# Kernel tuning notes

Hardware: AMD Instinct MI355X
Metric: run time of the kernel (lower is better)

## Reference

```python
import jax, jax.numpy as jnp
import numpy as np

EPS = 1e-15
PROJ_EPS = 1e-05


def project_hyp_vec(x):
    # clamp squared norm from below at 1 - PROJ_EPS (torch.clamp with min only)
    norm = jnp.sum(x * x, axis=-1, keepdims=True)
    return x * (1.0 - PROJ_EPS) / jnp.maximum(norm, 1.0 - PROJ_EPS)


def atanh(x):
    return 0.5 * jnp.log((1.0 + x) / (1.0 - x))


def mob_add(u, v):
    v = v + EPS
    norm_uv = 2.0 * jnp.sum(u * v, axis=-1, keepdims=True)
    norm_u = jnp.sum(u * u, axis=-1, keepdims=True)
    norm_v = jnp.sum(v * v, axis=-1, keepdims=True)
    denom = 1.0 + norm_uv + norm_v * norm_u
    result = (1.0 + norm_uv + norm_v) / denom * u + (1.0 - norm_u) / denom * v
    return project_hyp_vec(result)


def mob_mat_mul(M, x):
    x = project_hyp_vec(x)
    Mx = x @ M                                   # [B, H]
    Mx_norm = jnp.linalg.norm(Mx + EPS, axis=-1, keepdims=True)
    x_norm = jnp.linalg.norm(x + EPS, axis=-1, keepdims=True)
    return project_hyp_vec(jnp.tanh(Mx_norm / x_norm * atanh(x_norm)) / Mx_norm * Mx)


def setup_inputs() -> dict:
    key = jax.random.key(0)
    k_in, k_w, k_u = jax.random.split(key, 3)
    B, S, I, H = 256, 512, 256, 256
    inputs = jax.random.normal(k_in, (B, S, I), dtype=jnp.float32) * 0.1
    k = (1.0 / H) ** 0.5
    w = jax.random.uniform(k_w, (H, H), minval=-k, maxval=k, dtype=jnp.float32)
    u = jax.random.uniform(k_u, (I, H), minval=-k, maxval=k, dtype=jnp.float32)
    b = jnp.zeros((H,), dtype=jnp.float32)
    return {"inputs": inputs, "w": w, "u": u, "b": b}


def reference(inputs, w, u, b):
    B, S, I = inputs.shape
    H = w.shape[0]

    def step(h, x):
        Wh = mob_mat_mul(w, h)          # [B, H]
        Ux = mob_mat_mul(u, x)          # [B, H]
        h_new = mob_add(mob_add(Wh, Ux), b)
        return h_new, h_new

    h0 = jnp.zeros((B, H), dtype=inputs.dtype)
    _, outs = jax.lax.scan(step, h0, jnp.swapaxes(inputs, 0, 1))  # [S, B, H]
    return jnp.swapaxes(outs, 0, 1)  # [B, S, H]
```

## Files before the change

kernel.cpp:

```cpp
#include <hip/hip_runtime.h>

#define EPSV 1e-15f
#define PEPS 1e-5f

typedef float v2f __attribute__((ext_vector_type(2)));

__device__ __forceinline__ float frcp(float x) { return __builtin_amdgcn_rcpf(x); }
__device__ __forceinline__ float fexp2(float x) { return __builtin_amdgcn_exp2f(x); }
__device__ __forceinline__ float flog2(float x) { return __builtin_amdgcn_logf(x); }
__device__ __forceinline__ float projscale(float n2) {
  return n2 > (1.f - PEPS) ? (1.f - PEPS) * frcp(n2) : 1.f;
}

template <int CTRL>
__device__ __forceinline__ float dppadd(float x) {
  int y = __builtin_amdgcn_update_dpp(0, __float_as_int(x), CTRL, 0xF, 0xF, true);
  return x + __int_as_float(y);
}
__device__ __forceinline__ float wave_sum(float x) {
  x = dppadd<0x111>(x);
  x = dppadd<0x112>(x);
  x = dppadd<0x114>(x);
  x = dppadd<0x118>(x);
  x = dppadd<0x142>(x);
  x = dppadd<0x143>(x);
  return __int_as_float(__builtin_amdgcn_readlane(__float_as_int(x), 63));
}

__global__ __launch_bounds__(256) void ux_kernel(
    const float* __restrict__ x, const float* __restrict__ u,
    const float* __restrict__ bvec, float* __restrict__ out,
    float4* __restrict__ vstat, int use_vstat)
{
  __shared__ __align__(16) float xsT[256][36];

  const int tid = threadIdx.x;
  const int lane = tid & 63, wv = tid >> 6;
  const long long base = (long long)blockIdx.x * 32;

  #pragma unroll
  for (int k4 = 0; k4 < 8; ++k4) {
    float t0 = x[(base + k4 * 4 + 0) * 256 + tid];
    float t1 = x[(base + k4 * 4 + 1) * 256 + tid];
    float t2 = x[(base + k4 * 4 + 2) * 256 + tid];
    float t3 = x[(base + k4 * 4 + 3) * 256 + tid];
    float4 v; v.x = t0; v.y = t1; v.z = t2; v.w = t3;
    *reinterpret_cast<float4*>(&xsT[tid][k4 * 4]) = v;
  }
  __syncthreads();

  float4 bb = *reinterpret_cast<const float4*>(&bvec[4 * lane]);
  bb.x += EPSV; bb.y += EPSV; bb.z += EPSV; bb.w += EPSV;
  float S_vbrow = wave_sum(bb.x + bb.y + bb.z + bb.w);

  float s1[8], s2[8];
  #pragma unroll
  for (int r = 0; r < 8; ++r) { s1[r] = 0.f; s2[r] = 0.f; }
  #pragma unroll
  for (int c = 0; c < 4; ++c) {
    const int i = lane + 64 * c;
    float4 xa = *reinterpret_cast<const float4*>(&xsT[i][8 * wv]);
    float4 xb = *reinterpret_cast<const float4*>(&xsT[i][8 * wv + 4]);
    s1[0] += xa.x; s2[0] += xa.x * xa.x;
    s1[1] += xa.y; s2[1] += xa.y * xa.y;
    s1[2] += xa.z; s2[2] += xa.z * xa.z;
    s1[3] += xa.w; s2[3] += xa.w * xa.w;
    s1[4] += xb.x; s2[4] += xb.x * xb.x;
    s1[5] += xb.y; s2[5] += xb.y * xb.y;
    s1[6] += xb.z; s2[6] += xb.z * xb.z;
    s1[7] += xb.w; s2[7] += xb.w * xb.w;
  }
  float rs[8], xnr[8];
  #pragma unroll
  for (int r = 0; r < 8; ++r) {
    float a = wave_sum(s1[r]);
    float b2 = wave_sum(s2[r]);
    float sc = projscale(b2);
    rs[r] = sc;
    xnr[r] = sqrtf(sc * sc * b2 + 2.f * sc * EPSV * a + 256.f * EPSV * EPSV);
  }

  float4 acc[8];
  #pragma unroll
  for (int r = 0; r < 8; ++r) { acc[r].x = 0.f; acc[r].y = 0.f; acc[r].z = 0.f; acc[r].w = 0.f; }
  #pragma unroll 2
  for (int i = 0; i < 256; ++i) {
    float4 uv = *reinterpret_cast<const float4*>(&u[i * 256 + 4 * lane]);
    float4 xa = *reinterpret_cast<const float4*>(&xsT[i][8 * wv]);
    float4 xb = *reinterpret_cast<const float4*>(&xsT[i][8 * wv + 4]);
    acc[0].x += uv.x * xa.x; acc[0].y += uv.y * xa.x; acc[0].z += uv.z * xa.x; acc[0].w += uv.w * xa.x;
    acc[1].x += uv.x * xa.y; acc[1].y += uv.y * xa.y; acc[1].z += uv.z * xa.y; acc[1].w += uv.w * xa.y;
    acc[2].x += uv.x * xa.z; acc[2].y += uv.y * xa.z; acc[2].z += uv.z * xa.z; acc[2].w += uv.w * xa.z;
    acc[3].x += uv.x * xa.w; acc[3].y += uv.y * xa.w; acc[3].z += uv.z * xa.w; acc[3].w += uv.w * xa.w;
    acc[4].x += uv.x * xb.x; acc[4].y += uv.y * xb.x; acc[4].z += uv.z * xb.x; acc[4].w += uv.w * xb.x;
    acc[5].x += uv.x * xb.y; acc[5].y += uv.y * xb.y; acc[5].z += uv.z * xb.y; acc[5].w += uv.w * xb.y;
    acc[6].x += uv.x * xb.z; acc[6].y += uv.y * xb.z; acc[6].z += uv.z * xb.z; acc[6].w += uv.w * xb.z;
    acc[7].x += uv.x * xb.w; acc[7].y += uv.y * xb.w; acc[7].z += uv.z * xb.w; acc[7].w += uv.w * xb.w;
  }

  #pragma unroll
  for (int r = 0; r < 8; ++r) {
    float t1 = wave_sum(acc[r].x + acc[r].y + acc[r].z + acc[r].w);
    float t2 = wave_sum(acc[r].x * acc[r].x + acc[r].y * acc[r].y +
                        acc[r].z * acc[r].z + acc[r].w * acc[r].w);
    float t3 = wave_sum(acc[r].x * bb.x + acc[r].y * bb.y + acc[r].z * bb.z + acc[r].w * bb.w);
    float Sm  = rs[r] * t1;
    float Sm2 = rs[r] * rs[r] * t2;
    float mxn = sqrtf(Sm2 + 2.f * EPSV * Sm + 256.f * EPSV * EPSV);
    float xn = xnr[r];
    float at = 0.34657359f * flog2((1.f + xn) * frcp(1.f - xn));
    float arg = mxn * frcp(xn) * at;
    float e2 = fexp2(arg * 2.8853902f);
    float th = 1.f - 2.f * frcp(e2 + 1.f);
    float g = th * frcp(mxn);
    float fs = g * projscale(g * g * Sm2) * rs[r];
    float4 o;
    o.x = fs * acc[r].x + EPSV; o.y = fs * acc[r].y + EPSV;
    o.z = fs * acc[r].z + EPSV; o.w = fs * acc[r].w + EPSV;
    reinterpret_cast<float4*>(out)[(base + 8 * wv + r) * 64 + lane] = o;
    if (use_vstat && lane == 0) {
      float Sv  = fs * t1 + 256.f * EPSV;
      float Sv2 = fs * fs * t2 + 2.f * EPSV * fs * t1 + 256.f * EPSV * EPSV;
      float Svb = fs * t3 + EPSV * S_vbrow;
      vstat[base + 8 * wv + r] = float4{Sv, Sv2, Svb, 0.f};
    }
  }
}

template <int NR>
__device__ __forceinline__ void load_w(const float* __restrict__ w, int rb, int lane, v2f* wr) {
  #pragma unroll
  for (int r = 0; r < NR; ++r) {
    float4 t = *reinterpret_cast<const float4*>(&w[(rb + r) * 256 + 4 * lane]);
    asm volatile("" : "+v"(t.x), "+v"(t.y), "+v"(t.z), "+v"(t.w));
    wr[2 * r]     = v2f{t.x, t.y};
    wr[2 * r + 1] = v2f{t.z, t.w};
  }
}

template <int NR>
__device__ __forceinline__ void mv_pq(const v2f* wr, const float* mxp, const float* vp,
                                      float4& P, float4& Q) {
  v2f pl{0.f, 0.f}, ph{0.f, 0.f}, ql{0.f, 0.f}, qh{0.f, 0.f};
  #pragma unroll
  for (int i = 0; i < NR / 4; ++i) {
    float4 h4 = *reinterpret_cast<const float4*>(mxp + 4 * i);
    float4 u4 = *reinterpret_cast<const float4*>(vp + 4 * i);
    pl += wr[8 * i + 0] * h4.x; ph += wr[8 * i + 1] * h4.x;
    pl += wr[8 * i + 2] * h4.y; ph += wr[8 * i + 3] * h4.y;
    pl += wr[8 * i + 4] * h4.z; ph += wr[8 * i + 5] * h4.z;
    pl += wr[8 * i + 6] * h4.w; ph += wr[8 * i + 7] * h4.w;
    ql += wr[8 * i + 0] * u4.x; qh += wr[8 * i + 1] * u4.x;
    ql += wr[8 * i + 2] * u4.y; qh += wr[8 * i + 3] * u4.y;
    ql += wr[8 * i + 4] * u4.z; qh += wr[8 * i + 5] * u4.z;
    ql += wr[8 * i + 6] * u4.w; qh += wr[8 * i + 7] * u4.w;
  }
  P = float4{pl.x, pl.y, ph.x, ph.y};
  Q = float4{ql.x, ql.y, qh.x, qh.y};
}

__global__ __launch_bounds__(512, 1) void rnn_kernel(
    const float* __restrict__ w, const float* __restrict__ bvec,
    float* __restrict__ out, const float4* __restrict__ vstat, int S, int use_vstat)
{
  __shared__ __align__(16) float mx_lds[256];
  __shared__ __align__(16) float v_lds[2][256];
  __shared__ __align__(16) float pP[8][256];
  __shared__ __align__(16) float pQ[8][256];

  const int tid = threadIdx.x;
  const int lane = tid & 63;
  const int wv = tid >> 6;

  const long long rb4 = (long long)blockIdx.x * S * 64;
  const long long vsbase = (long long)blockIdx.x * S;
  const float4* outv = reinterpret_cast<const float4*>(out);
  float4* outw = reinterpret_cast<float4*>(out);
  const float4 zero4{0.f, 0.f, 0.f, 0.f};

  if (wv == 0) {
    v2f wr0[8];
    load_w<4>(w, 0, lane, wr0);

    float4 vb4 = *reinterpret_cast<const float4*>(&bvec[4 * lane]);
    vb4.x += EPSV; vb4.y += EPSV; vb4.z += EPSV; vb4.w += EPSV;
    float S_vb  = wave_sum(vb4.x + vb4.y + vb4.z + vb4.w);
    float S_vb2 = wave_sum(vb4.x * vb4.x + vb4.y * vb4.y + vb4.z * vb4.z + vb4.w * vb4.w);

    reinterpret_cast<float4*>(mx_lds)[lane] = zero4;
    reinterpret_cast<float4*>(v_lds[0])[lane] = vb4;
    __syncthreads();

    {
      float4 P, Q; mv_pq<4>(wr0, &mx_lds[0], &v_lds[0][0], P, Q);
      *reinterpret_cast<float4*>(&pP[0][4 * lane]) = P;
      *reinterpret_cast<float4*>(&pQ[0][4 * lane]) = Q;
    }
    __syncthreads();

    float4 Wvb4 = zero4;
    #pragma unroll
    for (int k = 0; k < 8; ++k) {
      float4 qq = *reinterpret_cast<const float4*>(&pQ[k][4 * lane]);
      Wvb4.x += qq.x; Wvb4.y += qq.y; Wvb4.z += qq.z; Wvb4.w += qq.w;
    }
    float4 vA = outv[rb4 + lane];
    float4 vB = outv[rb4 + 64 + lane];
    float4 sA = zero4, sB = zero4;
    if (use_vstat) { sA = vstat[vsbase]; sB = vstat[vsbase + 1]; }
    reinterpret_cast<float4*>(v_lds[0])[lane] = vA;
    __syncthreads();

    float4 m4 = zero4;
    float S_h = 0.f, S_h2 = 0.f;

    for (int t = 0; t < S; ++t) {
      const int b = t & 1;
      float4 v4 = vA;

      float S_Mx  = wave_sum(m4.x + m4.y + m4.z + m4.w);
      float S_Mx2 = wave_sum(m4.x * m4.x + m4.y * m4.y + m4.z * m4.z + m4.w * m4.w);
      float S_Mxv = wave_sum(m4.x * v4.x + m4.y * v4.y + m4.z * v4.z + m4.w * v4.w);
      float S_Mxb = wave_sum(m4.x * vb4.x + m4.y * vb4.y + m4.z * vb4.z + m4.w * vb4.w);
      float S_v, S_v2, S_vvb;
      if (use_vstat) { S_v = sA.x; S_v2 = sA.y; S_vvb = sA.z; }
      else {
        S_v   = wave_sum(v4.x + v4.y + v4.z + v4.w);
        S_v2  = wave_sum(v4.x * v4.x + v4.y * v4.y + v4.z * v4.z + v4.w * v4.w);
        S_vvb = wave_sum(v4.x * vb4.x + v4.y * vb4.y + v4.z * vb4.z + v4.w * vb4.w);
      }

      float s_hp = projscale(S_h2);
      float xn = sqrtf(s_hp * s_hp * S_h2 + 2.f * s_hp * EPSV * S_h + 256.f * EPSV * EPSV);
      float mxn = sqrtf(S_Mx2 + 2.f * EPSV * S_Mx + 256.f * EPSV * EPSV);
      float at = 0.34657359f * flog2((1.f + xn) * frcp(1.f - xn));
      float arg = mxn * frcp(xn) * at;
      float e2 = fexp2(arg * 2.8853902f);
      float th = 1.f - 2.f * frcp(e2 + 1.f);
      float g = th * frcp(mxn);
      float beta = g * projscale(g * g * S_Mx2);

      float nuv = 2.f * beta * S_Mxv;
      float nu  = beta * beta * S_Mx2;
      float nv  = S_v2;
      float rden = frcp(1.f + nuv + nv * nu);
      float cA = (1.f + nuv + nv) * rden;
      float cB = (1.f - nu) * rden;
      float cAb = cA * beta;
      float S_r1  = cAb * S_Mx + cB * S_v;
      float S_r12 = cAb * cAb * S_Mx2 + 2.f * cAb * cB * S_Mxv + cB * cB * S_v2;
      float S_r1b = cAb * S_Mxb + cB * S_vvb;
      float s1p = projscale(S_r12);
      float S_U = s1p * S_r1, S_U2 = s1p * s1p * S_r12, S_Ub = s1p * S_r1b;

      float nuv2 = 2.f * S_Ub;
      float rden2 = frcp(1.f + nuv2 + S_vb2 * S_U2);
      float dA = (1.f + nuv2 + S_vb2) * rden2;
      float dB = (1.f - S_U2) * rden2;
      float S_hn  = dA * S_U + dB * S_vb;
      float S_hn2 = dA * dA * S_U2 + 2.f * dA * dB * S_Ub + dB * dB * S_vb2;
      float s2p = projscale(S_hn2);

      float km = s2p * dA * s1p * cAb;
      float kv = s2p * dA * s1p * cB;
      float kb = s2p * dB;

      float4 hn{km * m4.x + kv * v4.x + kb * vb4.x,
                km * m4.y + kv * v4.y + kb * vb4.y,
                km * m4.z + kv * v4.z + kb * vb4.z,
                km * m4.w + kv * v4.w + kb * vb4.w};
      outw[rb4 + (long long)t * 64 + lane] = hn;

      S_h  = s2p * S_hn;
      S_h2 = s2p * s2p * S_hn2;
      float snextp = projscale(S_h2);

      if (t + 1 < S) reinterpret_cast<float4*>(v_lds[(t + 1) & 1])[lane] = vB;
      float4 vC = vB, sC = sB;
      if (t + 2 < S) {
        vC = outv[rb4 + (long long)(t + 2) * 64 + lane];
        if (use_vstat) sC = vstat[vsbase + t + 2];
      }

      {
        float4 P, Q; mv_pq<4>(wr0, &mx_lds[0], &v_lds[b][0], P, Q);
        *reinterpret_cast<float4*>(&pP[0][4 * lane]) = P;
        *reinterpret_cast<float4*>(&pQ[0][4 * lane]) = Q;
      }
      __syncthreads();

      float4 Pc = zero4, Qc = zero4;
      #pragma unroll
      for (int k = 0; k < 8; ++k) {
        float4 pp = *reinterpret_cast<const float4*>(&pP[k][4 * lane]);
        float4 qq = *reinterpret_cast<const float4*>(&pQ[k][4 * lane]);
        Pc.x += pp.x; Pc.y += pp.y; Pc.z += pp.z; Pc.w += pp.w;
        Qc.x += qq.x; Qc.y += qq.y; Qc.z += qq.z; Qc.w += qq.w;
      }
      m4.x = snextp * (km * Pc.x + kv * Qc.x + kb * Wvb4.x);
      m4.y = snextp * (km * Pc.y + kv * Qc.y + kb * Wvb4.y);
      m4.z = snextp * (km * Pc.z + kv * Qc.z + kb * Wvb4.z);
      m4.w = snextp * (km * Pc.w + kv * Qc.w + kb * Wvb4.w);
      reinterpret_cast<float4*>(mx_lds)[lane] = m4;
      __syncthreads();

      vA = vB; vB = vC; sA = sB; sB = sC;
    }
  } else {
    const int rb = 4 + (wv - 1) * 36;
    v2f wrk[72];
    load_w<36>(w, rb, lane, wrk);
    __syncthreads();
    {
      float4 P, Q; mv_pq<36>(wrk, &mx_lds[rb], &v_lds[0][rb], P, Q);
      *reinterpret_cast<float4*>(&pP[wv][4 * lane]) = P;
      *reinterpret_cast<float4*>(&pQ[wv][4 * lane]) = Q;
    }
    __syncthreads();
    __syncthreads();

    for (int t = 0; t < S; ++t) {
      const int b = t & 1;
      float4 P, Q;
      mv_pq<36>(wrk, &mx_lds[rb], &v_lds[b][rb], P, Q);
      *reinterpret_cast<float4*>(&pP[wv][4 * lane]) = P;
      *reinterpret_cast<float4*>(&pQ[wv][4 * lane]) = Q;
      __syncthreads();
      __syncthreads();
    }
  }
}

extern "C" void kernel_launch(void* const* d_in, const int* in_sizes, int n_in,
                              void* d_out, int out_size, void* d_ws, size_t ws_size,
                              hipStream_t stream) {
  const float* x = (const float*)d_in[0];
  const float* w = (const float*)d_in[1];
  const float* u = (const float*)d_in[2];
  const float* b = (const float*)d_in[3];
  float* out = (float*)d_out;

  const int nrows = in_sizes[0] / 256;
  const int S = 512;
  const int B = nrows / S;

  const int use_vstat = (ws_size >= (size_t)nrows * 16) ? 1 : 0;
  float4* vstat = (float4*)d_ws;

  ux_kernel<<<nrows / 32, 256, 0, stream>>>(x, u, b, out, vstat, use_vstat);
  rnn_kernel<<<B, 512, 0, stream>>>(w, b, out, vstat, S, use_vstat);
}
```

Baseline: 906.2 us.

## Split recurrent matvec across 16 waves and offload input prefetch to a helper wave

The recurrent kernel grows from 8 to 16 waves per block (1024 threads). Each worker wave now holds 16 or 20 rows of W in registers instead of 36, and wave 0 holds 8 rows, which shortens the per-step matvec critical path. Prefetching the next input rows into LDS moves from the serial wave 0 to wave 1, so wave 0 now reads v from LDS. The cost is a wider barrier across 16 waves, a 16-way partial-sum reduction in wave 0, and doubled LDS for partials.

```diff
diff --git a/kernel.cpp b/kernel.cpp
--- a/kernel.cpp
+++ b/kernel.cpp
@@ -159,14 +159,22 @@
   Q = float4{ql.x, ql.y, qh.x, qh.y};
 }
 
-__global__ __launch_bounds__(512, 1) void rnn_kernel(
+__device__ __forceinline__ int row_base(int wv) {
+  if (wv == 0) return 0;
+  if (wv <= 13) return 8 + (wv - 1) * 16;
+  return 216 + (wv - 14) * 20;
+}
+
+__global__ __launch_bounds__(1024)
+__attribute__((amdgpu_waves_per_eu(4, 4)))
+void rnn_kernel(
     const float* __restrict__ w, const float* __restrict__ bvec,
     float* __restrict__ out, const float4* __restrict__ vstat, int S, int use_vstat)
 {
   __shared__ __align__(16) float mx_lds[256];
   __shared__ __align__(16) float v_lds[2][256];
-  __shared__ __align__(16) float pP[8][256];
-  __shared__ __align__(16) float pQ[8][256];
+  __shared__ __align__(16) float pP[16][256];
+  __shared__ __align__(16) float pQ[16][256];
 
   const int tid = threadIdx.x;
   const int lane = tid & 63;
@@ -179,8 +187,8 @@
   const float4 zero4{0.f, 0.f, 0.f, 0.f};
 
   if (wv == 0) {
-    v2f wr0[8];
-    load_w<4>(w, 0, lane, wr0);
+    v2f wr[16];
+    load_w<8>(w, 0, lane, wr);
 
     float4 vb4 = *reinterpret_cast<const float4*>(&bvec[4 * lane]);
     vb4.x += EPSV; vb4.y += EPSV; vb4.z += EPSV; vb4.w += EPSV;
@@ -192,7 +200,7 @@
     __syncthreads();
 
     {
-      float4 P, Q; mv_pq<4>(wr0, &mx_lds[0], &v_lds[0][0], P, Q);
+      float4 P, Q; mv_pq<8>(wr, &mx_lds[0], &v_lds[0][0], P, Q);
       *reinterpret_cast<float4*>(&pP[0][4 * lane]) = P;
       *reinterpret_cast<float4*>(&pQ[0][4 * lane]) = Q;
     }
@@ -200,15 +208,12 @@
 
     float4 Wvb4 = zero4;
     #pragma unroll
-    for (int k = 0; k < 8; ++k) {
+    for (int k = 0; k < 16; ++k) {
       float4 qq = *reinterpret_cast<const float4*>(&pQ[k][4 * lane]);
       Wvb4.x += qq.x; Wvb4.y += qq.y; Wvb4.z += qq.z; Wvb4.w += qq.w;
     }
-    float4 vA = outv[rb4 + lane];
-    float4 vB = outv[rb4 + 64 + lane];
-    float4 sA = zero4, sB = zero4;
-    if (use_vstat) { sA = vstat[vsbase]; sB = vstat[vsbase + 1]; }
-    reinterpret_cast<float4*>(v_lds[0])[lane] = vA;
+    float sAx = 0.f, sAy = 0.f, sAz = 0.f;
+    if (use_vstat) { float4 s = vstat[vsbase]; sAx = s.x; sAy = s.y; sAz = s.z; }
     __syncthreads();
 
     float4 m4 = zero4;
@@ -216,14 +221,17 @@
 
     for (int t = 0; t < S; ++t) {
       const int b = t & 1;
-      float4 v4 = vA;
+      float nsx = 0.f, nsy = 0.f, nsz = 0.f;
+      if (use_vstat && t + 1 < S) { float4 s = vstat[vsbase + t + 1]; nsx = s.x; nsy = s.y; nsz = s.z; }
+
+      float4 v4 = *reinterpret_cast<const float4*>(&v_lds[b][4 * lane]);
 
       float S_Mx  = wave_sum(m4.x + m4.y + m4.z + m4.w);
       float S_Mx2 = wave_sum(m4.x * m4.x + m4.y * m4.y + m4.z * m4.z + m4.w * m4.w);
       float S_Mxv = wave_sum(m4.x * v4.x + m4.y * v4.y + m4.z * v4.z + m4.w * v4.w);
       float S_Mxb = wave_sum(m4.x * vb4.x + m4.y * vb4.y + m4.z * vb4.z + m4.w * vb4.w);
       float S_v, S_v2, S_vvb;
-      if (use_vstat) { S_v = sA.x; S_v2 = sA.y; S_vvb = sA.z; }
+      if (use_vstat) { S_v = sAx; S_v2 = sAy; S_vvb = sAz; }
       else {
         S_v   = wave_sum(v4.x + v4.y + v4.z + v4.w);
         S_v2  = wave_sum(v4.x * v4.x + v4.y * v4.y + v4.z * v4.z + v4.w * v4.w);
@@ -275,15 +283,8 @@
       S_h2 = s2p * s2p * S_hn2;
       float snextp = projscale(S_h2);
 
-      if (t + 1 < S) reinterpret_cast<float4*>(v_lds[(t + 1) & 1])[lane] = vB;
-      float4 vC = vB, sC = sB;
-      if (t + 2 < S) {
-        vC = outv[rb4 + (long long)(t + 2) * 64 + lane];
-        if (use_vstat) sC = vstat[vsbase + t + 2];
-      }
-
       {
-        float4 P, Q; mv_pq<4>(wr0, &mx_lds[0], &v_lds[b][0], P, Q);
+        float4 P, Q; mv_pq<8>(wr, &mx_lds[0], &v_lds[b][0], P, Q);
         *reinterpret_cast<float4*>(&pP[0][4 * lane]) = P;
         *reinterpret_cast<float4*>(&pQ[0][4 * lane]) = Q;
       }
@@ -291,7 +292,7 @@
 
       float4 Pc = zero4, Qc = zero4;
       #pragma unroll
-      for (int k = 0; k < 8; ++k) {
+      for (int k = 0; k < 16; ++k) {
         float4 pp = *reinterpret_cast<const float4*>(&pP[k][4 * lane]);
         float4 qq = *reinterpret_cast<const float4*>(&pQ[k][4 * lane]);
         Pc.x += pp.x; Pc.y += pp.y; Pc.z += pp.z; Pc.w += pp.w;
@@ -304,29 +305,80 @@
       reinterpret_cast<float4*>(mx_lds)[lane] = m4;
       __syncthreads();
 
-      vA = vB; vB = vC; sA = sB; sB = sC;
-    }
-  } else {
-    const int rb = 4 + (wv - 1) * 36;
-    v2f wrk[72];
-    load_w<36>(w, rb, lane, wrk);
+      sAx = nsx; sAy = nsy; sAz = nsz;
+    }
+  } else if (wv == 1) {
+    v2f wr[32];
+    const int rb = row_base(1);
+    load_w<16>(w, rb, lane, wr);
+
+    float4 vA = outv[rb4 + lane];
+    float4 vB = outv[rb4 + 64 + lane];
+    float4 vC = outv[rb4 + 128 + lane];
     __syncthreads();
     {
-      float4 P, Q; mv_pq<36>(wrk, &mx_lds[rb], &v_lds[0][rb], P, Q);
-      *reinterpret_cast<float4*>(&pP[wv][4 * lane]) = P;
-      *reinterpret_cast<float4*>(&pQ[wv][4 * lane]) = Q;
-    }
-    __syncthreads();
+      float4 P, Q; mv_pq<16>(wr, &mx_lds[rb], &v_lds[0][rb], P, Q);
+      *reinterpret_cast<float4*>(&pP[1][4 * lane]) = P;
+      *reinterpret_cast<float4*>(&pQ[1][4 * lane]) = Q;
+    }
+    __syncthreads();
+    reinterpret_cast<float4*>(v_lds[0])[lane] = vA;
     __syncthreads();
 
     for (int t = 0; t < S; ++t) {
       const int b = t & 1;
       float4 P, Q;
-      mv_pq<36>(wrk, &mx_lds[rb], &v_lds[b][rb], P, Q);
-      *reinterpret_cast<float4*>(&pP[wv][4 * lane]) = P;
-      *reinterpret_cast<float4*>(&pQ[wv][4 * lane]) = Q;
-      __syncthreads();
-      __syncthreads();
+      mv_pq<16>(wr, &mx_lds[rb], &v_lds[b][rb], P, Q);
+      *reinterpret_cast<float4*>(&pP[1][4 * lane]) = P;
+      *reinterpret_cast<float4*>(&pQ[1][4 * lane]) = Q;
+      if (t + 1 < S) reinterpret_cast<float4*>(v_lds[(t + 1) & 1])[lane] = vB;
+      vB = vC;
+      if (t + 3 < S) vC = outv[rb4 + (long long)(t + 3) * 64 + lane];
+      __syncthreads();
+      __syncthreads();
+    }
+  } else {
+    const int rb = row_base(wv);
+    if (wv >= 14) {
+      v2f wr[40];
+      load_w<20>(w, rb, lane, wr);
+      __syncthreads();
+      {
+        float4 P, Q; mv_pq<20>(wr, &mx_lds[rb], &v_lds[0][rb], P, Q);
+        *reinterpret_cast<float4*>(&pP[wv][4 * lane]) = P;
+        *reinterpret_cast<float4*>(&pQ[wv][4 * lane]) = Q;
+      }
+      __syncthreads();
+      __syncthreads();
+      for (int t = 0; t < S; ++t) {
+        const int b = t & 1;
+        float4 P, Q;
+        mv_pq<20>(wr, &mx_lds[rb], &v_lds[b][rb], P, Q);
+        *reinterpret_cast<float4*>(&pP[wv][4 * lane]) = P;
+        *reinterpret_cast<float4*>(&pQ[wv][4 * lane]) = Q;
+        __syncthreads();
+        __syncthreads();
+      }
+    } else {
+      v2f wr[32];
+      load_w<16>(w, rb, lane, wr);
+      __syncthreads();
+      {
+        float4 P, Q; mv_pq<16>(wr, &mx_lds[rb], &v_lds[0][rb], P, Q);
+        *reinterpret_cast<float4*>(&pP[wv][4 * lane]) = P;
+        *reinterpret_cast<float4*>(&pQ[wv][4 * lane]) = Q;
+      }
+      __syncthreads();
+      __syncthreads();
+      for (int t = 0; t < S; ++t) {
+        const int b = t & 1;
+        float4 P, Q;
+        mv_pq<16>(wr, &mx_lds[rb], &v_lds[b][rb], P, Q);
+        *reinterpret_cast<float4*>(&pP[wv][4 * lane]) = P;
+        *reinterpret_cast<float4*>(&pQ[wv][4 * lane]) = Q;
+        __syncthreads();
+        __syncthreads();
+      }
     }
   }
 }
@@ -348,5 +400,5 @@
   float4* vstat = (float4*)d_ws;
 
   ux_kernel<<<nrows / 32, 256, 0, stream>>>(x, u, b, out, vstat, use_vstat);
-  rnn_kernel<<<B, 512, 0, stream>>>(w, b, out, vstat, S, use_vstat);
-}
+  rnn_kernel<<<B, 1024, 0, stream>>>(w, b, out, vstat, S, use_vstat);
+}
```

Result: slower. 963.7 us (+6.3%).
